# Performance work log

Measured on AMD Instinct MI355X. Metric: run time of the kernel, lower is better.

## Reference

```python
import jax, jax.numpy as jnp
import numpy as np

B, NPG, H, D = 8, 6250, 4, 128   # graphs, nodes/graph, heads, hidden
N = B * NPG                       # 50000 nodes total
E = 400000                        # edges
VOCAB = 10000


def setup_inputs() -> dict:
    key = jax.random.key(0)
    ks = jax.random.split(key, 12)
    p = lambda k, shape: jax.random.normal(k, shape, dtype=jnp.float32) * 0.05
    return {
        "node_ids": jax.random.randint(ks[0], (N,), 0, VOCAB),
        "src": jax.random.randint(ks[1], (E,), 0, N),
        "dst": jax.random.randint(ks[2], (E,), 0, N),
        "emb": p(ks[3], (VOCAB, D)),
        "W_src": p(ks[4], (D, H * D)), "b_src": jnp.zeros((H * D,), jnp.float32),
        "W_dst": p(ks[5], (D, H * D)), "b_dst": jnp.zeros((H * D,), jnp.float32),
        "attn": p(ks[6], (H, D)),
        "W_res": p(ks[7], (D, H * D)), "b_res": jnp.zeros((H * D,), jnp.float32),
        "W_gc": p(ks[8], (D, D)), "b_gc": jnp.zeros((D,), jnp.float32),
        "W_mlp": p(ks[9], (3 * D, 1)), "b_mlp": jnp.zeros((1,), jnp.float32),
    }


def _leaky(x, s):
    return jnp.where(x >= 0, x, s * x)


def _maxpool(feat):
    # dgl.max_nodes: per-graph max over nodes -> [B, feat_dim]
    return jnp.max(feat.reshape(B, NPG, -1), axis=1)


def _gatv2(x, src, dst, W_src, b_src, W_dst, b_dst, attn, W_res, b_res):
    # DGL GATv2Conv (share_weights=False, residual=True, eval mode -> no dropout)
    hs = (x @ W_src + b_src).reshape(N, H, D)
    hd = (x @ W_dst + b_dst).reshape(N, H, D)
    e = _leaky(hs[src] + hd[dst], 0.2)              # [E,H,D]
    logits = jnp.einsum('ehd,hd->eh', e, attn)      # [E,H]
    m = jax.ops.segment_max(logits, dst, num_segments=N)
    ex = jnp.exp(logits - m[dst])
    denom = jax.ops.segment_sum(ex, dst, num_segments=N)
    alpha = ex / denom[dst]                          # edge softmax per dst/head
    rst = jax.ops.segment_sum(hs[src] * alpha[..., None], dst, num_segments=N)
    rst = rst + (x @ W_res + b_res).reshape(N, H, D)
    return _leaky(rst, 0.01)                         # nn.LeakyReLU() activation


def _graphconv(x, src, dst, W, b):
    # DGL GraphConv norm='both', allow_zero_in_degree=True, LeakyReLU activation
    ones = jnp.ones((E,), x.dtype)
    dout = jnp.clip(jax.ops.segment_sum(ones, src, num_segments=N), 1.0, None)
    din = jnp.clip(jax.ops.segment_sum(ones, dst, num_segments=N), 1.0, None)
    h = x * jax.lax.rsqrt(dout)[:, None]
    agg = jax.ops.segment_sum(h[src], dst, num_segments=N)
    h = agg * jax.lax.rsqrt(din)[:, None]
    return _leaky(h @ W + b, 0.01)


def reference(node_ids, src, dst, emb, W_src, b_src, W_dst, b_dst, attn,
              W_res, b_res, W_gc, b_gc, W_mlp, b_mlp):
    feat = emb[node_ids]                             # featurize_nodes
    pools = [_maxpool(feat)]
    res = _gatv2(feat, src, dst, W_src, b_src, W_dst, b_dst, attn,
                 W_res, b_res).mean(axis=1)          # mean over heads -> [N,D]
    pools.append(_maxpool(res))
    res = _graphconv(res, src, dst, W_gc, b_gc)
    pools.append(_maxpool(res))
    agg = jnp.concatenate(pools, axis=1)             # [B, 3D]
    # reward_predictor_block_two: ReLU -> (Dropout eval) -> Linear(3D, 1)
    return jax.nn.relu(agg) @ W_mlp + b_mlp          # BCE logits [B,1]
```

## Files before the change

kernel.cpp:

```cpp
#include <hip/hip_runtime.h>
#include <float.h>
#include <math.h>

#define Bg   8
#define NPGc 6250
#define Hh   4
#define Dd   128
#define Nn   50000
#define Ee   400000
#define HDd  512
#define WNf  1536
#define NCHUNK 49

typedef unsigned short ushort_t;
typedef __attribute__((ext_vector_type(8))) short bf16x8;
typedef __attribute__((ext_vector_type(4))) float f32x4;
typedef __attribute__((ext_vector_type(2))) float f32x2;
typedef __attribute__((ext_vector_type(4))) unsigned u32x4;

__device__ __forceinline__ void atomicMaxF(float* addr, float val) {
    if (val >= 0.0f) atomicMax((int*)addr, __float_as_int(val));
    else             atomicMin((unsigned int*)addr, __float_as_uint(val));
}

__device__ __forceinline__ ushort_t f2bf(float x) {
    unsigned u = __float_as_uint(x);
    unsigned r = (u + 0x7FFFu + ((u >> 16) & 1u)) >> 16;
    return (ushort_t)r;
}

__device__ __forceinline__ f32x2 bfpair(unsigned u) {
    f32x2 r;
    r.x = __uint_as_float(u << 16);
    r.y = __uint_as_float(u & 0xFFFF0000u);
    return r;
}

__global__ void setup_kernel(const int* __restrict__ ids, const float* __restrict__ emb,
                             ushort_t* __restrict__ feat_bf,
                             const int* __restrict__ src, const int* __restrict__ dst,
                             const float* __restrict__ W_src, const float* __restrict__ W_dst,
                             const float* __restrict__ W_res, const float* __restrict__ W_gc,
                             const float* __restrict__ b_src, const float* __restrict__ b_dst,
                             const float* __restrict__ b_res,
                             ushort_t* __restrict__ Wt, ushort_t* __restrict__ Wt_gc,
                             float* __restrict__ bias_f,
                             int* __restrict__ din_i, float* __restrict__ dout,
                             float* __restrict__ pools) {
    int i = blockIdx.x * blockDim.x + threadIdx.x;
    {
        int n = i >> 5, c = i & 31;
        int id = ids[n];
        float4 v = ((const float4*)emb)[(size_t)id * 32 + c];
        ushort4 b;
        b.x = f2bf(v.x); b.y = f2bf(v.y); b.z = f2bf(v.z); b.w = f2bf(v.w);
        ((ushort4*)feat_bf)[(size_t)n * 32 + c] = b;
    }
    if (i < Ee) {
        atomicAdd(&din_i[dst[i]], 1);
        atomicAdd(&dout[src[i]], 1.0f);
    }
    if (i < Bg * 3 * Dd) pools[i] = -FLT_MAX;
    if (i < WNf * 128) {
        int c = i >> 7, k = i & 127;
        float v = (c < 512) ? W_src[k * 512 + c]
                : (c < 1024) ? W_dst[k * 512 + (c - 512)]
                             : W_res[k * 512 + (c - 1024)];
        Wt[i] = f2bf(v);
    } else if (i < WNf * 128 + 128 * 128) {
        int j = i - WNf * 128;
        int c = j >> 7, k = j & 127;
        Wt_gc[j] = f2bf(W_gc[k * 128 + c]);
    }
    if (i < WNf)
        bias_f[i] = (i < 512) ? b_src[i] : (i < 1024) ? b_dst[i - 512] : b_res[i - 1024];
}

__global__ void maxpool_bf_kernel(const ushort_t* __restrict__ x, float* __restrict__ pools, int col_off) {
    int b = blockIdx.x, chunk = blockIdx.y, lane = threadIdx.x;
    int i0 = chunk * 125;
    f32x2 mx = {-FLT_MAX, -FLT_MAX};
    for (int i = 0; i < 125; ++i) {
        unsigned u = *(const unsigned*)(x + ((size_t)(b * NPGc + i0 + i)) * Dd + lane * 2);
        mx = __builtin_elementwise_max(mx, bfpair(u));
    }
    atomicMaxF(&pools[b * (3 * Dd) + col_off + lane * 2],     mx.x);
    atomicMaxF(&pools[b * (3 * Dd) + col_off + lane * 2 + 1], mx.y);
}

#define GNT 3
#define NCS 8
__global__ __launch_bounds__(256) void mfma_gemm_kernel(
    const ushort_t* __restrict__ A, const ushort_t* __restrict__ Wt,
    const float* __restrict__ bias, ushort_t* __restrict__ Ohs,
    ushort_t* __restrict__ Odr, int n_rows)
{
    __shared__ ushort_t Cs[2][64 * 64];
    int bid = blockIdx.x;
    int lin = (bid & 7) * (gridDim.x >> 3) + (bid >> 3);
    int row0 = (lin / NCS) * 64;
    int ct0  = (lin % NCS) * GNT;
    int w = threadIdx.x >> 6, lane = threadIdx.x & 63;
    int lrow = lane & 15, kg = lane >> 4;

    bf16x8 av[4][4];
    {
        const ushort_t* ap = A + (size_t)(row0 + lrow) * 128 + kg * 8;
        #pragma unroll
        for (int fi = 0; fi < 4; ++fi)
            #pragma unroll
            for (int ks = 0; ks < 4; ++ks)
                av[fi][ks] = *(const bf16x8*)(ap + fi * 16 * 128 + ks * 32);
    }
    bf16x8 wv[GNT][4];
    float4 bv[GNT];
    {
        const ushort_t* wp = Wt + (size_t)(ct0 * 64 + w * 16 + lrow) * 128 + kg * 8;
        #pragma unroll
        for (int ct = 0; ct < GNT; ++ct) {
            #pragma unroll
            for (int ks = 0; ks < 4; ++ks)
                wv[ct][ks] = *(const bf16x8*)(wp + (size_t)ct * 8192 + ks * 32);
            bv[ct] = *(const float4*)(bias + (ct0 + ct) * 64 + w * 16 + kg * 4);
        }
    }

    #pragma unroll
    for (int ct = 0; ct < GNT; ++ct) {
        f32x4 acc[4] = {};
        #pragma unroll
        for (int ks = 0; ks < 4; ++ks)
            #pragma unroll
            for (int fi = 0; fi < 4; ++fi)
                acc[fi] = __builtin_amdgcn_mfma_f32_16x16x32_bf16(wv[ct][ks], av[fi][ks], acc[fi], 0, 0, 0);

        ushort_t* cb = Cs[ct & 1];
        int cbase = w * 32 + kg * 8;
        #pragma unroll
        for (int fi = 0; fi < 4; ++fi) {
            float o0 = acc[fi][0] + bv[ct].x;
            float o1 = acc[fi][1] + bv[ct].y;
            float o2 = acc[fi][2] + bv[ct].z;
            float o3 = acc[fi][3] + bv[ct].w;
            unsigned q0, q1;
            asm("v_cvt_pk_bf16_f32 %0, %1, %2" : "=v"(q0) : "v"(o0), "v"(o1));
            asm("v_cvt_pk_bf16_f32 %0, %1, %2" : "=v"(q1) : "v"(o2), "v"(o3));
            int r = fi * 16 + lrow;
            int cbyte = cbase ^ ((r & 7) << 4);
            uint2 q; q.x = q0; q.y = q1;
            *(uint2*)((char*)cb + r * 128 + cbyte) = q;
        }
        __syncthreads();
        {
            int t = threadIdx.x;
            const char* cbr = (const char*)cb;
            int gcol = (ct0 + ct) * 64;
            char* ob; int wn;
            if (gcol < 512) { ob = (char*)Ohs; wn = 512; }
            else            { ob = (char*)Odr; wn = 1024; gcol -= 512; }
            #pragma unroll
            for (int h = 0; h < 2; ++h) {
                int r  = (h * 256 + t) >> 3;
                int ch = t & 7;
                int cbyte = (ch * 16) ^ ((r & 7) << 4);
                u32x4 v = *(const u32x4*)(cbr + r * 128 + cbyte);
                int grow = row0 + r;
                if (grow < n_rows)
                    *(u32x4*)(ob + ((size_t)grow * wn + gcol) * 2 + ch * 16) = v;
            }
        }
    }
}

__global__ __launch_bounds__(256) void mfma_gc_pool_kernel(
    const ushort_t* __restrict__ A, const ushort_t* __restrict__ Wt,
    const float* __restrict__ bias, float* __restrict__ pools)
{
    int g = blockIdx.x / 98, lb = blockIdx.x % 98;
    int row0 = g * NPGc + lb * 64;
    int w = threadIdx.x >> 6, lane = threadIdx.x & 63;
    int lrow = lane & 15, kg = lane >> 4;

    bf16x8 av[4][4];
    {
        const ushort_t* ap = A + (size_t)(row0 + lrow) * 128 + kg * 8;
        #pragma unroll
        for (int fi = 0; fi < 4; ++fi)
            #pragma unroll
            for (int ks = 0; ks < 4; ++ks)
                av[fi][ks] = *(const bf16x8*)(ap + fi * 16 * 128 + ks * 32);
    }

    #pragma unroll
    for (int ct = 0; ct < 2; ++ct) {
        bf16x8 wv[4];
        const ushort_t* wp = Wt + (size_t)(ct * 64 + w * 16 + lrow) * 128 + kg * 8;
        #pragma unroll
        for (int ks = 0; ks < 4; ++ks) wv[ks] = *(const bf16x8*)(wp + ks * 32);

        f32x4 acc[4] = {};
        #pragma unroll
        for (int ks = 0; ks < 4; ++ks)
            #pragma unroll
            for (int fi = 0; fi < 4; ++fi)
                acc[fi] = __builtin_amdgcn_mfma_f32_16x16x32_bf16(wv[ks], av[fi][ks], acc[fi], 0, 0, 0);

        int colb = ct * 64 + w * 16 + kg * 4;
        float4 bv4 = *(const float4*)(bias + colb);
        float mcol[4] = {-FLT_MAX, -FLT_MAX, -FLT_MAX, -FLT_MAX};
        #pragma unroll
        for (int fi = 0; fi < 4; ++fi) {
            int lr = lb * 64 + fi * 16 + lrow;
            bool valid = lr < NPGc;
            #pragma unroll
            for (int j = 0; j < 4; ++j) {
                float v = acc[fi][j] + ((const float*)&bv4)[j];
                v = v >= 0.0f ? v : 0.01f * v;
                if (valid) mcol[j] = fmaxf(mcol[j], v);
            }
        }
        #pragma unroll
        for (int j = 0; j < 4; ++j) {
            mcol[j] = fmaxf(mcol[j], __shfl_xor(mcol[j], 1));
            mcol[j] = fmaxf(mcol[j], __shfl_xor(mcol[j], 2));
            mcol[j] = fmaxf(mcol[j], __shfl_xor(mcol[j], 4));
            mcol[j] = fmaxf(mcol[j], __shfl_xor(mcol[j], 8));
        }
        if (lrow == 0) {
            #pragma unroll
            for (int j = 0; j < 4; ++j)
                atomicMaxF(&pools[g * (3 * Dd) + 2 * Dd + colb + j], mcol[j]);
        }
    }
}

__global__ __launch_bounds__(256) void scan_reduce_kernel(const int* __restrict__ din_i,
                                                          int* __restrict__ partials) {
    int b = blockIdx.x, t = threadIdx.x;
    int base = b * 1024 + t * 4;
    int s = 0;
    #pragma unroll
    for (int j = 0; j < 4; ++j) { int i = base + j; if (i < Nn) s += din_i[i]; }
    #pragma unroll
    for (int off = 32; off > 0; off >>= 1) s += __shfl_xor(s, off);
    __shared__ int wsum[4];
    if ((t & 63) == 0) wsum[t >> 6] = s;
    __syncthreads();
    if (t == 0) partials[b] = wsum[0] + wsum[1] + wsum[2] + wsum[3];
}

__global__ void scan_mid_kernel(int* __restrict__ partials, int* __restrict__ row_start) {
    if (threadIdx.x == 0) {
        int acc = 0;
        for (int i = 0; i < NCHUNK; ++i) { int v = partials[i]; partials[i] = acc; acc += v; }
        row_start[Nn] = acc;
    }
}

__global__ __launch_bounds__(256) void scan_final_kernel(const int* __restrict__ din_i,
                                                         const int* __restrict__ partials,
                                                         int* __restrict__ row_start,
                                                         float* __restrict__ din_f) {
    int b = blockIdx.x, t = threadIdx.x;
    int base = b * 1024 + t * 4;
    int v[4]; int s = 0;
    #pragma unroll
    for (int j = 0; j < 4; ++j) {
        v[j] = (base + j < Nn) ? din_i[base + j] : 0;
        s += v[j];
    }
    __shared__ int buf[256];
    buf[t] = s;
    __syncthreads();
    #pragma unroll
    for (int off = 1; off < 256; off <<= 1) {
        int x = (t >= off) ? buf[t - off] : 0;
        __syncthreads();
        buf[t] += x;
        __syncthreads();
    }
    int excl = buf[t] - s + partials[b];
    #pragma unroll
    for (int j = 0; j < 4; ++j) {
        if (base + j < Nn) {
            row_start[base + j] = excl;
            din_f[base + j] = (float)v[j];
            excl += v[j];
        }
    }
}

__global__ void scatter_kernel(const int* __restrict__ src, const int* __restrict__ dst,
                               const int* __restrict__ row_start, int* __restrict__ cursor,
                               int* __restrict__ csr_src) {
    int e = blockIdx.x * blockDim.x + threadIdx.x;
    if (e >= Ee) return;
    int d = dst[e];
    int slot = row_start[d] + atomicAdd(&cursor[d], 1);
    csr_src[slot] = src[e];
}

__global__ __launch_bounds__(256) void gat_fused_kernel(
    const ushort_t* __restrict__ hs, const ushort_t* __restrict__ hdres,
    const float* __restrict__ attn,
    const int* __restrict__ row_start, const int* __restrict__ csr_src,
    ushort_t* __restrict__ res_bf)
{
    int d = (blockIdx.x * 256 + threadIdx.x) >> 6;
    int lane = threadIdx.x & 63;
    if (d >= Nn) return;
    int e0 = row_start[d], e1 = row_start[d + 1];

    const f32x2 z2 = {0.0f, 0.0f};
    f32x2 hd0, hd1, hd2, hd3, at0, at1, at2, at3;
    {
        u32x4 hr = __builtin_nontemporal_load((const u32x4*)(hdres + (size_t)d * 1024 + lane * 8));
        hd0 = bfpair(hr.x); hd1 = bfpair(hr.y); hd2 = bfpair(hr.z); hd3 = bfpair(hr.w);
        float4 a0 = *(const float4*)(attn + lane * 8);
        float4 a1 = *(const float4*)(attn + lane * 8 + 4);
        at0.x = a0.x; at0.y = a0.y; at1.x = a0.z; at1.y = a0.w;
        at2.x = a1.x; at2.y = a1.y; at3.x = a1.z; at3.y = a1.w;
    }

    float denom = 0.0f;
    f32x2 ac0 = z2, ac1 = z2, ac2 = z2, ac3 = z2;

#define LOGIT_PRE(rr, h0, h1, h2, h3, pout)                                           \
    {                                                                                 \
        h0 = bfpair(rr.x); h1 = bfpair(rr.y); h2 = bfpair(rr.z); h3 = bfpair(rr.w);   \
        f32x2 p2 = z2;                                                                \
        { f32x2 x = h0 + hd0;                                                         \
          p2 += (__builtin_elementwise_max(x, z2) + 0.2f * __builtin_elementwise_min(x, z2)) * at0; } \
        { f32x2 x = h1 + hd1;                                                         \
          p2 += (__builtin_elementwise_max(x, z2) + 0.2f * __builtin_elementwise_min(x, z2)) * at1; } \
        { f32x2 x = h2 + hd2;                                                         \
          p2 += (__builtin_elementwise_max(x, z2) + 0.2f * __builtin_elementwise_min(x, z2)) * at2; } \
        { f32x2 x = h3 + hd3;                                                         \
          p2 += (__builtin_elementwise_max(x, z2) + 0.2f * __builtin_elementwise_min(x, z2)) * at3; } \
        pout = p2.x + p2.y;                                                           \
    }

    int e = e0;
    for (; e + 4 <= e1; e += 4) {
        int sA = csr_src[e], sB = csr_src[e + 1], sC = csr_src[e + 2], sD = csr_src[e + 3];
        uint4 rA = *(const uint4*)(hs + (size_t)sA * HDd + lane * 8);
        uint4 rB = *(const uint4*)(hs + (size_t)sB * HDd + lane * 8);
        uint4 rC = *(const uint4*)(hs + (size_t)sC * HDd + lane * 8);
        uint4 rD = *(const uint4*)(hs + (size_t)sD * HDd + lane * 8);
        f32x2 hA0, hA1, hA2, hA3, hB0, hB1, hB2, hB3;
        f32x2 hC0, hC1, hC2, hC3, hD0, hD1, hD2, hD3;
        float pA, pB, pC, pD;
        LOGIT_PRE(rA, hA0, hA1, hA2, hA3, pA);
        LOGIT_PRE(rB, hB0, hB1, hB2, hB3, pB);
        LOGIT_PRE(rC, hC0, hC1, hC2, hC3, pC);
        LOGIT_PRE(rD, hD0, hD1, hD2, hD3, pD);
        pA += __shfl_xor(pA, 1); pB += __shfl_xor(pB, 1); pC += __shfl_xor(pC, 1); pD += __shfl_xor(pD, 1);
        pA += __shfl_xor(pA, 2); pB += __shfl_xor(pB, 2); pC += __shfl_xor(pC, 2); pD += __shfl_xor(pD, 2);
        pA += __shfl_xor(pA, 4); pB += __shfl_xor(pB, 4); pC += __shfl_xor(pC, 4); pD += __shfl_xor(pD, 4);
        pA += __shfl_xor(pA, 8); pB += __shfl_xor(pB, 8); pC += __shfl_xor(pC, 8); pD += __shfl_xor(pD, 8);
        float exA = __expf(fminf(fmaxf(pA, -40.0f), 40.0f));
        float exB = __expf(fminf(fmaxf(pB, -40.0f), 40.0f));
        float exC = __expf(fminf(fmaxf(pC, -40.0f), 40.0f));
        float exD = __expf(fminf(fmaxf(pD, -40.0f), 40.0f));
        denom += (exA + exB) + (exC + exD);
        ac0 += hA0 * exA + hB0 * exB + hC0 * exC + hD0 * exD;
        ac1 += hA1 * exA + hB1 * exB + hC1 * exC + hD1 * exD;
        ac2 += hA2 * exA + hB2 * exB + hC2 * exC + hD2 * exD;
        ac3 += hA3 * exA + hB3 * exB + hC3 * exC + hD3 * exD;
    }
    for (; e < e1; ++e) {
        int s = csr_src[e];
        uint4 rr = *(const uint4*)(hs + (size_t)s * HDd + lane * 8);
        f32x2 h0, h1, h2, h3;
        float p;
        LOGIT_PRE(rr, h0, h1, h2, h3, p);
        p += __shfl_xor(p, 1); p += __shfl_xor(p, 2);
        p += __shfl_xor(p, 4); p += __shfl_xor(p, 8);
        float ex = __expf(fminf(fmaxf(p, -40.0f), 40.0f));
        denom += ex;
        ac0 += h0 * ex; ac1 += h1 * ex; ac2 += h2 * ex; ac3 += h3 * ex;
    }
#undef LOGIT_PRE

    float inv = (e1 > e0) ? 1.0f / denom : 0.0f;
    f32x2 rv0, rv1, rv2, rv3;
    {
        u32x4 rr = __builtin_nontemporal_load((const u32x4*)(hdres + (size_t)d * 1024 + 512 + lane * 8));
        rv0 = bfpair(rr.x); rv1 = bfpair(rr.y); rv2 = bfpair(rr.z); rv3 = bfpair(rr.w);
    }
    float t[8];
    {
        f32x2 v0 = ac0 * inv + rv0, v1 = ac1 * inv + rv1;
        f32x2 v2 = ac2 * inv + rv2, v3 = ac3 * inv + rv3;
        f32x2 l0 = __builtin_elementwise_max(v0, z2) + 0.01f * __builtin_elementwise_min(v0, z2);
        f32x2 l1 = __builtin_elementwise_max(v1, z2) + 0.01f * __builtin_elementwise_min(v1, z2);
        f32x2 l2 = __builtin_elementwise_max(v2, z2) + 0.01f * __builtin_elementwise_min(v2, z2);
        f32x2 l3 = __builtin_elementwise_max(v3, z2) + 0.01f * __builtin_elementwise_min(v3, z2);
        t[0] = l0.x; t[1] = l0.y; t[2] = l1.x; t[3] = l1.y;
        t[4] = l2.x; t[5] = l2.y; t[6] = l3.x; t[7] = l3.y;
    }
    #pragma unroll
    for (int j = 0; j < 8; ++j) {
        t[j] += __shfl_xor(t[j], 16);
        t[j] += __shfl_xor(t[j], 32);
    }
    if (lane < 16) {
        float o0 = 0.25f * t[0], o1 = 0.25f * t[1], o2 = 0.25f * t[2], o3 = 0.25f * t[3];
        float o4 = 0.25f * t[4], o5 = 0.25f * t[5], o6 = 0.25f * t[6], o7 = 0.25f * t[7];
        unsigned q0, q1, q2, q3;
        asm("v_cvt_pk_bf16_f32 %0, %1, %2" : "=v"(q0) : "v"(o0), "v"(o1));
        asm("v_cvt_pk_bf16_f32 %0, %1, %2" : "=v"(q1) : "v"(o2), "v"(o3));
        asm("v_cvt_pk_bf16_f32 %0, %1, %2" : "=v"(q2) : "v"(o4), "v"(o5));
        asm("v_cvt_pk_bf16_f32 %0, %1, %2" : "=v"(q3) : "v"(o6), "v"(o7));
        uint4 qb; qb.x = q0; qb.y = q1; qb.z = q2; qb.w = q3;
        *(uint4*)(res_bf + (size_t)d * Dd + lane * 8) = qb;
    }
}

__global__ __launch_bounds__(256) void gc_gather_kernel(
    const ushort_t* __restrict__ res_bf, const int* __restrict__ row_start,
    const int* __restrict__ csr_src, const float* __restrict__ dout,
    const float* __restrict__ din, ushort_t* __restrict__ agg_bf)
{
    int d = (blockIdx.x * 256 + threadIdx.x) >> 6;
    int lane = threadIdx.x & 63;
    if (d >= Nn) return;
    int e0 = row_start[d], e1 = row_start[d + 1];
    const f32x2 z2 = {0.0f, 0.0f};
    f32x2 a2 = z2;
    int e = e0;
    for (; e + 4 <= e1; e += 4) {
        int s0 = csr_src[e],     s1 = csr_src[e + 1];
        int s2 = csr_src[e + 2], s3 = csr_src[e + 3];
        float c0 = 1.0f / sqrtf(fmaxf(dout[s0], 1.0f));
        float c1 = 1.0f / sqrtf(fmaxf(dout[s1], 1.0f));
        float c2 = 1.0f / sqrtf(fmaxf(dout[s2], 1.0f));
        float c3 = 1.0f / sqrtf(fmaxf(dout[s3], 1.0f));
        unsigned u0 = *(const unsigned*)(res_bf + (size_t)s0 * Dd + lane * 2);
        unsigned u1 = *(const unsigned*)(res_bf + (size_t)s1 * Dd + lane * 2);
        unsigned u2 = *(const unsigned*)(res_bf + (size_t)s2 * Dd + lane * 2);
        unsigned u3 = *(const unsigned*)(res_bf + (size_t)s3 * Dd + lane * 2);
        a2 += bfpair(u0) * c0 + bfpair(u1) * c1 + bfpair(u2) * c2 + bfpair(u3) * c3;
    }
    for (; e < e1; ++e) {
        int s = csr_src[e];
        float c = 1.0f / sqrtf(fmaxf(dout[s], 1.0f));
        unsigned u = *(const unsigned*)(res_bf + (size_t)s * Dd + lane * 2);
        a2 += bfpair(u) * c;
    }
    float scd = 1.0f / sqrtf(fmaxf(din[d], 1.0f));
    float ax = a2.x * scd, ay = a2.y * scd;
    unsigned q;
    asm("v_cvt_pk_bf16_f32 %0, %1, %2" : "=v"(q) : "v"(ax), "v"(ay));
    *(unsigned*)(agg_bf + (size_t)d * Dd + lane * 2) = q;
}

__global__ void final_kernel(const float* __restrict__ pools, const float* __restrict__ W_mlp,
                             const float* __restrict__ b_mlp, float* __restrict__ out) {
    int b = blockIdx.x, lane = threadIdx.x;
    float s = 0.0f;
    for (int j = lane; j < 3 * Dd; j += 64)
        s += fmaxf(pools[b * (3 * Dd) + j], 0.0f) * W_mlp[j];
    #pragma unroll
    for (int off = 32; off > 0; off >>= 1) s += __shfl_xor(s, off);
    if (lane == 0) out[b] = s + b_mlp[0];
}

extern "C" void kernel_launch(void* const* d_in, const int* in_sizes, int n_in,
                              void* d_out, int out_size, void* d_ws, size_t ws_size,
                              hipStream_t stream) {
    const int*   node_ids = (const int*)d_in[0];
    const int*   src      = (const int*)d_in[1];
    const int*   dst      = (const int*)d_in[2];
    const float* emb      = (const float*)d_in[3];
    const float* W_src    = (const float*)d_in[4];
    const float* b_src    = (const float*)d_in[5];
    const float* W_dst    = (const float*)d_in[6];
    const float* b_dst    = (const float*)d_in[7];
    const float* attn     = (const float*)d_in[8];
    const float* W_res    = (const float*)d_in[9];
    const float* b_res    = (const float*)d_in[10];
    const float* W_gc     = (const float*)d_in[11];
    const float* b_gc     = (const float*)d_in[12];
    const float* W_mlp    = (const float*)d_in[13];
    const float* b_mlp    = (const float*)d_in[14];
    float* out = (float*)d_out;

    char* w = (char*)d_ws;
    size_t off = 0;
    ushort_t* feat_bf = (ushort_t*)(w + off); off += (size_t)(Nn + 64) * Dd * 2;
    ushort_t* hs_buf  = (ushort_t*)(w + off); off += (size_t)Nn * HDd * 2;
    ushort_t* hdres   = (ushort_t*)(w + off); off += (size_t)Nn * 1024 * 2;
    ushort_t* Wt      = (ushort_t*)(w + off); off += (size_t)WNf * 128 * 2;
    ushort_t* Wt_gc   = (ushort_t*)(w + off); off += (size_t)128 * 128 * 2;
    float*    bias_f  = (float*)(w + off);    off += (size_t)WNf * 4;
    int*      csr_src = (int*)(w + off);      off += (size_t)Ee * 4;
    int*      row_st  = (int*)(w + off);      off += ((size_t)Nn + 4) * 4;
    int*      cursor  = (int*)(w + off);      off += (size_t)Nn * 4;
    int*      din_i   = (int*)(w + off);      off += (size_t)Nn * 4;
    float*    dout_f  = (float*)(w + off);    off += (size_t)Nn * 4;
    float*    din_f   = (float*)(w + off);    off += (size_t)Nn * 4;
    int*      partials= (int*)(w + off);      off += 64 * 4;
    float*    pools   = (float*)(w + off);    off += (size_t)Bg * 3 * Dd * 4;
    ushort_t* res_bf  = (ushort_t*)(w + off); off += (size_t)Nn * Dd * 2;

    ushort_t* agg_bf = hs_buf;

    hipMemsetAsync(cursor, 0, (size_t)3 * Nn * 4, stream);

    setup_kernel<<<(Nn * 32) / 256, 256, 0, stream>>>(
        node_ids, emb, feat_bf, src, dst, W_src, W_dst, W_res, W_gc,
        b_src, b_dst, b_res, Wt, Wt_gc, bias_f,
        din_i, dout_f, pools);
    maxpool_bf_kernel<<<dim3(Bg, 50), 64, 0, stream>>>(feat_bf, pools, 0);

    scan_reduce_kernel<<<NCHUNK, 256, 0, stream>>>(din_i, partials);
    scan_mid_kernel<<<1, 64, 0, stream>>>(partials, row_st);
    scan_final_kernel<<<NCHUNK, 256, 0, stream>>>(din_i, partials, row_st, din_f);
    scatter_kernel<<<(Ee + 255) / 256, 256, 0, stream>>>(src, dst, row_st, cursor, csr_src);

    mfma_gemm_kernel<<<((Nn + 63) / 64) * NCS, 256, 0, stream>>>(
        feat_bf, Wt, bias_f, hs_buf, hdres, Nn);

    gat_fused_kernel<<<(Nn * 64) / 256, 256, 0, stream>>>(
        hs_buf, hdres, attn, row_st, csr_src, res_bf);
    maxpool_bf_kernel<<<dim3(Bg, 50), 64, 0, stream>>>(res_bf, pools, Dd);

    gc_gather_kernel<<<(Nn * 64) / 256, 256, 0, stream>>>(res_bf, row_st, csr_src, dout_f, din_f, agg_bf);
    mfma_gc_pool_kernel<<<Bg * 98, 256, 0, stream>>>(agg_bf, Wt_gc, b_gc, pools);

    final_kernel<<<Bg, 64, 0, stream>>>(pools, W_mlp, b_mlp, out);
}
```

Before: 336.4 us.

## Merge three-pass degree scan into one block kernel and unroll gather by eight

Replaces the reduce/mid/final three-kernel prefix scan over in-degrees with a single 1024-thread block in which each thread scans 49 contiguous entries, removing two kernel launches and their dependencies. The GraphConv gather loop is also unrolled from 4 to 8 edges per iteration, with the loads batched, to raise memory-level parallelism. The single-block scan does strided, uncoalesced per-thread reads on one CU, and the wider unroll increases register use.

```diff
diff --git a/kernel.cpp b/kernel.cpp
--- a/kernel.cpp
+++ b/kernel.cpp
@@ -10,7 +10,6 @@
 #define Ee   400000
 #define HDd  512
 #define WNf  1536
-#define NCHUNK 49
 
 typedef unsigned short ushort_t;
 typedef __attribute__((ext_vector_type(8))) short bf16x8;
@@ -234,60 +233,38 @@
     }
 }
 
-__global__ __launch_bounds__(256) void scan_reduce_kernel(const int* __restrict__ din_i,
-                                                          int* __restrict__ partials) {
-    int b = blockIdx.x, t = threadIdx.x;
-    int base = b * 1024 + t * 4;
+#define CPT 49
+__global__ __launch_bounds__(1024) void scan_kernel(const int* __restrict__ din_i,
+                                                    int* __restrict__ row_start,
+                                                    float* __restrict__ din_f) {
+    __shared__ int buf[1024];
+    int t = threadIdx.x;
+    int base = t * CPT;
     int s = 0;
-    #pragma unroll
-    for (int j = 0; j < 4; ++j) { int i = base + j; if (i < Nn) s += din_i[i]; }
-    #pragma unroll
-    for (int off = 32; off > 0; off >>= 1) s += __shfl_xor(s, off);
-    __shared__ int wsum[4];
-    if ((t & 63) == 0) wsum[t >> 6] = s;
-    __syncthreads();
-    if (t == 0) partials[b] = wsum[0] + wsum[1] + wsum[2] + wsum[3];
-}
-
-__global__ void scan_mid_kernel(int* __restrict__ partials, int* __restrict__ row_start) {
-    if (threadIdx.x == 0) {
-        int acc = 0;
-        for (int i = 0; i < NCHUNK; ++i) { int v = partials[i]; partials[i] = acc; acc += v; }
-        row_start[Nn] = acc;
-    }
-}
-
-__global__ __launch_bounds__(256) void scan_final_kernel(const int* __restrict__ din_i,
-                                                         const int* __restrict__ partials,
-                                                         int* __restrict__ row_start,
-                                                         float* __restrict__ din_f) {
-    int b = blockIdx.x, t = threadIdx.x;
-    int base = b * 1024 + t * 4;
-    int v[4]; int s = 0;
-    #pragma unroll
-    for (int j = 0; j < 4; ++j) {
-        v[j] = (base + j < Nn) ? din_i[base + j] : 0;
-        s += v[j];
-    }
-    __shared__ int buf[256];
+    for (int j = 0; j < CPT; ++j) {
+        int i = base + j;
+        if (i < Nn) s += din_i[i];
+    }
     buf[t] = s;
     __syncthreads();
     #pragma unroll
-    for (int off = 1; off < 256; off <<= 1) {
+    for (int off = 1; off < 1024; off <<= 1) {
         int x = (t >= off) ? buf[t - off] : 0;
         __syncthreads();
         buf[t] += x;
         __syncthreads();
     }
-    int excl = buf[t] - s + partials[b];
-    #pragma unroll
-    for (int j = 0; j < 4; ++j) {
-        if (base + j < Nn) {
-            row_start[base + j] = excl;
-            din_f[base + j] = (float)v[j];
-            excl += v[j];
-        }
-    }
+    int excl = buf[t] - s;
+    for (int j = 0; j < CPT; ++j) {
+        int i = base + j;
+        if (i < Nn) {
+            int v = din_i[i];
+            row_start[i] = excl;
+            din_f[i] = (float)v;
+            excl += v;
+        }
+    }
+    if (t == 1023) row_start[Nn] = buf[1023];
 }
 
 __global__ void scatter_kernel(const int* __restrict__ src, const int* __restrict__ dst,
@@ -429,18 +406,16 @@
     const f32x2 z2 = {0.0f, 0.0f};
     f32x2 a2 = z2;
     int e = e0;
-    for (; e + 4 <= e1; e += 4) {
-        int s0 = csr_src[e],     s1 = csr_src[e + 1];
-        int s2 = csr_src[e + 2], s3 = csr_src[e + 3];
-        float c0 = 1.0f / sqrtf(fmaxf(dout[s0], 1.0f));
-        float c1 = 1.0f / sqrtf(fmaxf(dout[s1], 1.0f));
-        float c2 = 1.0f / sqrtf(fmaxf(dout[s2], 1.0f));
-        float c3 = 1.0f / sqrtf(fmaxf(dout[s3], 1.0f));
-        unsigned u0 = *(const unsigned*)(res_bf + (size_t)s0 * Dd + lane * 2);
-        unsigned u1 = *(const unsigned*)(res_bf + (size_t)s1 * Dd + lane * 2);
-        unsigned u2 = *(const unsigned*)(res_bf + (size_t)s2 * Dd + lane * 2);
-        unsigned u3 = *(const unsigned*)(res_bf + (size_t)s3 * Dd + lane * 2);
-        a2 += bfpair(u0) * c0 + bfpair(u1) * c1 + bfpair(u2) * c2 + bfpair(u3) * c3;
+    for (; e + 8 <= e1; e += 8) {
+        int s[8]; float c[8]; unsigned u[8];
+        #pragma unroll
+        for (int k = 0; k < 8; ++k) s[k] = csr_src[e + k];
+        #pragma unroll
+        for (int k = 0; k < 8; ++k) c[k] = 1.0f / sqrtf(fmaxf(dout[s[k]], 1.0f));
+        #pragma unroll
+        for (int k = 0; k < 8; ++k) u[k] = *(const unsigned*)(res_bf + (size_t)s[k] * Dd + lane * 2);
+        #pragma unroll
+        for (int k = 0; k < 8; ++k) a2 += bfpair(u[k]) * c[k];
     }
     for (; e < e1; ++e) {
         int s = csr_src[e];
@@ -500,7 +475,6 @@
     int*      din_i   = (int*)(w + off);      off += (size_t)Nn * 4;
     float*    dout_f  = (float*)(w + off);    off += (size_t)Nn * 4;
     float*    din_f   = (float*)(w + off);    off += (size_t)Nn * 4;
-    int*      partials= (int*)(w + off);      off += 64 * 4;
     float*    pools   = (float*)(w + off);    off += (size_t)Bg * 3 * Dd * 4;
     ushort_t* res_bf  = (ushort_t*)(w + off); off += (size_t)Nn * Dd * 2;
 
@@ -514,9 +488,7 @@
         din_i, dout_f, pools);
     maxpool_bf_kernel<<<dim3(Bg, 50), 64, 0, stream>>>(feat_bf, pools, 0);
 
-    scan_reduce_kernel<<<NCHUNK, 256, 0, stream>>>(din_i, partials);
-    scan_mid_kernel<<<1, 64, 0, stream>>>(partials, row_st);
-    scan_final_kernel<<<NCHUNK, 256, 0, stream>>>(din_i, partials, row_st, din_f);
+    scan_kernel<<<1, 1024, 0, stream>>>(din_i, row_st, din_f);
     scatter_kernel<<<(Ee + 255) / 256, 256, 0, stream>>>(src, dst, row_st, cursor, csr_src);
 
     mfma_gemm_kernel<<<((Nn + 63) / 64) * NCS, 256, 0, stream>>>(
```

Result: slower. 452.6 us (+34.6%).
